# Kernel optimization log

Measured on AMD Instinct MI355X. Metric: run time of the kernel, lower is better.

## Reference

```python
import jax, jax.numpy as jnp
import numpy as np

HIDDEN = 2048
N_HEADS = 32
N_KV_HEADS = 8
HEAD_DIM = HIDDEN // N_HEADS  # 64
GROUPS = N_HEADS // N_KV_HEADS  # 4
ROPE_THETA = 10000.0
B, S = 1, 2048


def setup_inputs() -> dict:
    key = jax.random.key(0)
    ks = jax.random.split(key, 5)
    scale = 1.0 / np.sqrt(HIDDEN)
    return {
        "hidden_states": jax.random.normal(ks[0], (B, S, HIDDEN), dtype=jnp.float32),
        "Wq": jax.random.normal(ks[1], (HIDDEN, N_HEADS * HEAD_DIM), dtype=jnp.float32) * scale,
        "Wk": jax.random.normal(ks[2], (HIDDEN, N_KV_HEADS * HEAD_DIM), dtype=jnp.float32) * scale,
        "Wv": jax.random.normal(ks[3], (HIDDEN, N_KV_HEADS * HEAD_DIM), dtype=jnp.float32) * scale,
        "Wo": jax.random.normal(ks[4], (N_HEADS * HEAD_DIM, HIDDEN), dtype=jnp.float32) * scale,
    }


def _rope_tables(seq_len, dtype):
    # freqs_cos/sin buffers: [seq_len, HEAD_DIM//2]
    inv_freq = 1.0 / (ROPE_THETA ** (jnp.arange(0, HEAD_DIM, 2, dtype=jnp.float32) / HEAD_DIM))
    t = jnp.arange(seq_len, dtype=jnp.float32)
    freqs = jnp.outer(t, inv_freq)
    return jnp.cos(freqs).astype(dtype), jnp.sin(freqs).astype(dtype)


def _apply_rope(x, cos, sin):
    # x: [B, H, S, Dh], interleaved even/odd rotation
    xe = x[..., 0::2]
    xo = x[..., 1::2]
    # cos/sin: [S, Dh/2] -> broadcast over batch & heads
    out_e = xe * cos - xo * sin
    out_o = xe * sin + xo * cos
    return jnp.stack([out_e, out_o], axis=-1).reshape(x.shape)


def reference(hidden_states, Wq, Wk, Wv, Wo):
    bsz, q_len, _ = hidden_states.shape
    dtype = hidden_states.dtype

    q = (hidden_states @ Wq).reshape(bsz, q_len, N_HEADS, HEAD_DIM).transpose(0, 2, 1, 3)
    k = (hidden_states @ Wk).reshape(bsz, q_len, N_KV_HEADS, HEAD_DIM).transpose(0, 2, 1, 3)
    v = (hidden_states @ Wv).reshape(bsz, q_len, N_KV_HEADS, HEAD_DIM).transpose(0, 2, 1, 3)

    cos, sin = _rope_tables(q_len, dtype)
    q = _apply_rope(q, cos, sin)
    k = _apply_rope(k, cos, sin)

    # GQA: repeat_interleave kv heads to match query heads
    k = jnp.repeat(k, GROUPS, axis=1)  # [B, H, S, Dh]
    v = jnp.repeat(v, GROUPS, axis=1)

    # attention_mask=None path: no mask applied (matches module default)
    scores = jnp.einsum("bhqd,bhkd->bhqk", q, k) / jnp.sqrt(jnp.asarray(HEAD_DIM, dtype))
    attn = jax.nn.softmax(scores.astype(jnp.float32), axis=-1).astype(dtype)
    out = jnp.einsum("bhqk,bhkd->bhqd", attn, v)
    out = out.transpose(0, 2, 1, 3).reshape(bsz, q_len, N_HEADS * HEAD_DIM)
    return out @ Wo
```

## Files before the change

kernel.cpp:

```cpp
#include <hip/hip_runtime.h>

typedef __bf16 bf16x8 __attribute__((ext_vector_type(8)));
typedef float f32x4 __attribute__((ext_vector_type(4)));
typedef unsigned short u16x4 __attribute__((ext_vector_type(4)));
typedef unsigned short u16x8 __attribute__((ext_vector_type(8)));
typedef unsigned int u32x4 __attribute__((ext_vector_type(4)));

__device__ __forceinline__ float bf2f(unsigned short h) {
    union { unsigned int u; float f; } v;
    v.u = ((unsigned int)h) << 16;
    return v.f;
}
__device__ __forceinline__ unsigned short f2bf(float f) {
    return __builtin_bit_cast(unsigned short, (__bf16)f);
}
__device__ __forceinline__ void glds16(const unsigned short* g, unsigned short* l) {
    __builtin_amdgcn_global_load_lds((__attribute__((address_space(1))) void*)g,
                                     (__attribute__((address_space(3))) void*)l,
                                     16, 0, 0);
}

#define MFMA16(a, b, c) __builtin_amdgcn_mfma_f32_16x16x32_bf16((a), (b), (c), 0, 0, 0)

__global__ __launch_bounds__(256) void prep1(const float* __restrict__ X,
                                             const float* __restrict__ Wq,
                                             const float* __restrict__ Wk,
                                             const float* __restrict__ Wv,
                                             unsigned short* __restrict__ Xbf,
                                             unsigned short* __restrict__ wqkvT) {
    const int b = blockIdx.x;
    const int tid = threadIdx.x;
    if (b < 4096) {
        const int i = (b * 256 + tid) * 4;
        const float4 v = *(const float4*)(X + i);
        u16x4 o;
        o[0] = f2bf(v.x); o[1] = f2bf(v.y); o[2] = f2bf(v.z); o[3] = f2bf(v.w);
        *(u16x4*)(Xbf + i) = o;
        return;
    }
    __shared__ __align__(16) unsigned short tile[32][33];
    const int tx = tid & 31, ty = tid >> 5;
    const int b2 = b - 4096;
    const int kb = (b2 & 63) * 32;
    const int nb = (b2 >> 6) * 32;
    const float* src; int scol, sld;
    if (nb < 2048)      { src = Wq; scol = nb;        sld = 2048; }
    else if (nb < 2560) { src = Wk; scol = nb - 2048; sld = 512;  }
    else                { src = Wv; scol = nb - 2560; sld = 512;  }
#pragma unroll
    for (int i = 0; i < 32; i += 8)
        tile[ty + i][tx] = f2bf(src[(size_t)(kb + ty + i) * sld + (scol + tx)]);
    __syncthreads();
#pragma unroll
    for (int i = 0; i < 32; i += 8)
        wqkvT[(size_t)(nb + ty + i) * 2048 + (kb + tx)] = tile[tx][ty + i];
}

__global__ __launch_bounds__(256) void prep2(const float* __restrict__ Wo,
                                             const unsigned short* __restrict__ qkv,
                                             unsigned short* __restrict__ woT,
                                             unsigned short* __restrict__ vt) {
    const int b = blockIdx.x;
    const int tid = threadIdx.x;
    const int tx = tid & 31, ty = tid >> 5;
    __shared__ __align__(16) unsigned short tile[32][33];
    if (b < 4096) {
        const int kb = (b & 63) * 32;
        const int nb = (b >> 6) * 32;
#pragma unroll
        for (int i = 0; i < 32; i += 8)
            tile[ty + i][tx] = f2bf(Wo[(size_t)(kb + ty + i) * 2048 + (nb + tx)]);
        __syncthreads();
#pragma unroll
        for (int i = 0; i < 32; i += 8)
            woT[(size_t)(nb + ty + i) * 2048 + (kb + tx)] = tile[tx][ty + i];
    } else {
        const int b2 = b - 4096;
        const int bx = (b2 & 15) * 32;
        const int by = (b2 >> 4) * 32;
#pragma unroll
        for (int i = 0; i < 32; i += 8)
            tile[ty + i][tx] = qkv[(size_t)(by + ty + i) * 3072 + 2560 + bx + tx];
        __syncthreads();
#pragma unroll
        for (int i = 0; i < 32; i += 8)
            vt[(size_t)(bx + ty + i) * 2048 + (by + tx)] = tile[tx][ty + i];
    }
}

__global__ __launch_bounds__(256) void gemm128_qkv(const unsigned short* __restrict__ A,
                                                   const unsigned short* __restrict__ BT,
                                                   unsigned short* __restrict__ C) {
    __shared__ __align__(16) unsigned short As[128 * 64];
    __shared__ __align__(16) unsigned short Bs[128 * 64];

    const int tid = threadIdx.x;
    const int lane = tid & 63;
    const int wave = tid >> 6;
    const int quad = lane >> 4;
    const int l15 = lane & 15;
    const int bm = blockIdx.x * 128;
    const int bn = blockIdx.y * 128;
    const int wm = (wave & 1) * 64;
    const int wn = (wave >> 1) * 64;

    const int srow = wave * 8 + (lane >> 3);
    const int sw8 = (lane & 7) ^ (srow & 7);
    const unsigned short* Ag = A + (size_t)(bm + srow) * 2048 + sw8 * 8;
    const unsigned short* Bg = BT + (size_t)(bn + srow) * 2048 + sw8 * 8;
    unsigned short* Asl = As + wave * 512;
    unsigned short* Bsl = Bs + wave * 512;

    f32x4 acc[4][4] = {};

    for (int k0 = 0; k0 < 2048; k0 += 64) {
#pragma unroll
        for (int i = 0; i < 4; i++) {
            glds16(Ag + (size_t)(32 * i) * 2048 + k0, Asl + i * 2048);
            glds16(Bg + (size_t)(32 * i) * 2048 + k0, Bsl + i * 2048);
        }
        __syncthreads();
#pragma unroll
        for (int ks = 0; ks < 2; ks++) {
            bf16x8 af[4], bfr[4];
#pragma unroll
            for (int mt = 0; mt < 4; mt++) {
                const int row = wm + 16 * mt + l15;
                af[mt] = __builtin_bit_cast(bf16x8,
                    *(const u32x4*)&As[row * 64 + (((quad + 4 * ks) ^ (row & 7)) * 8)]);
            }
#pragma unroll
            for (int nt = 0; nt < 4; nt++) {
                const int row = wn + 16 * nt + l15;
                bfr[nt] = __builtin_bit_cast(bf16x8,
                    *(const u32x4*)&Bs[row * 64 + (((quad + 4 * ks) ^ (row & 7)) * 8)]);
            }
#pragma unroll
            for (int mt = 0; mt < 4; mt++)
#pragma unroll
                for (int nt = 0; nt < 4; nt++)
                    acc[mt][nt] = MFMA16(af[mt], bfr[nt], acc[mt][nt]);
        }
        __syncthreads();
    }

#pragma unroll
    for (int mt = 0; mt < 4; mt++) {
#pragma unroll
        for (int nt = 0; nt < 4; nt++) {
            const int col = bn + wn + 16 * nt + l15;
            if (col < 2560) {
                const int i = (col & 63) >> 1;
                const float inv = exp2f(-0.41524101186092036f * (float)i);
                const float sign = (col & 1) ? 1.0f : -1.0f;
#pragma unroll
                for (int r = 0; r < 4; r++) {
                    const int row = bm + wm + 16 * mt + quad * 4 + r;
                    float sn, cs;
                    __sincosf((float)row * inv, &sn, &cs);
                    const float partner = __shfl_xor(acc[mt][nt][r], 1, 64);
                    acc[mt][nt][r] = acc[mt][nt][r] * cs + sign * partner * sn;
                }
            }
#pragma unroll
            for (int r = 0; r < 4; r++) {
                const int row = bm + wm + 16 * mt + quad * 4 + r;
                C[(size_t)row * 3072 + col] = f2bf(acc[mt][nt][r]);
            }
        }
    }
}

template <int BM, bool ROPE>
__global__ __launch_bounds__(256) void gemm_bt(const unsigned short* __restrict__ A,
                                               const unsigned short* __restrict__ BT,
                                               void* __restrict__ Cv,
                                               int K, int lda, int ldb, int ldc,
                                               int out_f32) {
    constexpr int MT = BM / 32;
    constexpr int ACALLS = BM / 16;
    __shared__ __align__(16) unsigned short As[BM * 128];
    __shared__ __align__(16) unsigned short Bs[128 * 128];

    const int tid = threadIdx.x;
    const int lane = tid & 63;
    const int wave = tid >> 6;
    const int quad = lane >> 4;
    const int l15 = lane & 15;
    const int bm = blockIdx.x * BM;
    const int bn = blockIdx.y * 128;
    const int wm = (wave & 1) * (BM / 2);
    const int wn = (wave >> 1) * 64;

    const int srow = wave * 4 + (lane >> 4);
    const int sw = (lane & 15) ^ (srow & 7);
    const unsigned short* Ag = A + (size_t)(bm + srow) * lda + sw * 8;
    const unsigned short* Bg = BT + (size_t)(bn + srow) * ldb + sw * 8;
    unsigned short* Asl = As + wave * 512;
    unsigned short* Bsl = Bs + wave * 512;

    f32x4 acc[MT][4] = {};

    for (int k0 = 0; k0 < K; k0 += 128) {
#pragma unroll
        for (int i = 0; i < ACALLS; i++)
            glds16(Ag + (size_t)(16 * i) * lda + k0, Asl + i * 2048);
#pragma unroll
        for (int i = 0; i < 8; i++)
            glds16(Bg + (size_t)(16 * i) * ldb + k0, Bsl + i * 2048);
        __syncthreads();
#pragma unroll
        for (int ks = 0; ks < 4; ks++) {
            bf16x8 af[MT], bfr[4];
#pragma unroll
            for (int mt = 0; mt < MT; mt++) {
                const int row = wm + 16 * mt + l15;
                af[mt] = __builtin_bit_cast(bf16x8,
                    *(const u32x4*)&As[row * 128 + (((quad + 4 * ks) ^ (row & 7)) * 8)]);
            }
#pragma unroll
            for (int nt = 0; nt < 4; nt++) {
                const int row = wn + 16 * nt + l15;
                bfr[nt] = __builtin_bit_cast(bf16x8,
                    *(const u32x4*)&Bs[row * 128 + (((quad + 4 * ks) ^ (row & 7)) * 8)]);
            }
#pragma unroll
            for (int mt = 0; mt < MT; mt++)
#pragma unroll
                for (int nt = 0; nt < 4; nt++)
                    acc[mt][nt] = MFMA16(af[mt], bfr[nt], acc[mt][nt]);
        }
        __syncthreads();
    }

    if (ROPE) {
#pragma unroll
        for (int mt = 0; mt < MT; mt++) {
#pragma unroll
            for (int nt = 0; nt < 4; nt++) {
                const int col = bn + wn + 16 * nt + l15;
                if (col < 2560) {
                    const int i = (col & 63) >> 1;
                    const float inv = exp2f(-0.41524101186092036f * (float)i);
                    const float sign = (col & 1) ? 1.0f : -1.0f;
#pragma unroll
                    for (int r = 0; r < 4; r++) {
                        const int row = bm + wm + 16 * mt + quad * 4 + r;
                        float sn, cs;
                        __sincosf((float)row * inv, &sn, &cs);
                        const float partner = __shfl_xor(acc[mt][nt][r], 1, 64);
                        acc[mt][nt][r] = acc[mt][nt][r] * cs + sign * partner * sn;
                    }
                }
            }
        }
    }

#pragma unroll
    for (int mt = 0; mt < MT; mt++) {
#pragma unroll
        for (int nt = 0; nt < 4; nt++) {
#pragma unroll
            for (int r = 0; r < 4; r++) {
                const int row = bm + wm + 16 * mt + quad * 4 + r;
                const int col = bn + wn + 16 * nt + l15;
                if (out_f32)
                    ((float*)Cv)[(size_t)row * ldc + col] = acc[mt][nt][r];
                else
                    ((unsigned short*)Cv)[(size_t)row * ldc + col] = f2bf(acc[mt][nt][r]);
            }
        }
    }
}

__global__ __launch_bounds__(256) void attn_kernel(const unsigned short* __restrict__ qkv,
                                                   const unsigned short* __restrict__ vt,
                                                   unsigned short* __restrict__ attn_out) {
    const int qb = blockIdx.x;
    const int h = blockIdx.y;
    const int kvh = h >> 2;
    const int tid = threadIdx.x;
    const int lane = tid & 63;
    const int wave = tid >> 6;
    const int quad = lane >> 4;
    const int l15 = lane & 15;
    const int l7 = l15 & 7;
    const int w0 = qb * 64 + wave * 16;

    __shared__ __align__(16) unsigned short Ks[128 * 64];
    __shared__ __align__(16) unsigned short Vs[64 * 128];
    __shared__ __align__(16) unsigned short St[4][16][64];
    unsigned short (*Sw)[64] = St[wave];

    const int srow = wave * 8 + (lane >> 3);
    const int swK = (lane & 7) ^ (srow & 7);
    const unsigned short* Kg = qkv + 2048 + kvh * 64 + swK * 8;
    unsigned short* Ksl = Ks + wave * 512;
    const int vrow = wave * 4 + (lane >> 4);
    const int swV = (lane & 15) ^ (vrow & 7);
    const unsigned short* Vg = vt + (size_t)(kvh * 64 + vrow) * 2048 + swV * 8;
    unsigned short* Vsl = Vs + wave * 512;

    const float QSCALE = 0.18033688011111093f;
    bf16x8 qf[2];
#pragma unroll
    for (int ks = 0; ks < 2; ks++) {
        u32x4 raw = *(const u32x4*)&qkv[(size_t)(w0 + l15) * 3072 + h * 64 + quad * 8 + 32 * ks];
        u16x8 t = __builtin_bit_cast(u16x8, raw);
#pragma unroll
        for (int j = 0; j < 8; j++) t[j] = f2bf(bf2f(t[j]) * QSCALE);
        qf[ks] = __builtin_bit_cast(bf16x8, t);
    }

    bf16x8 ones;
#pragma unroll
    for (int j = 0; j < 8; j++) ones[j] = (__bf16)1.0f;

    f32x4 acc_o[4] = {};
    f32x4 acc_l = {};

    for (int kb2 = 0; kb2 < 16; kb2++) {
        const int kbase = kb2 * 128;
#pragma unroll
        for (int i = 0; i < 4; i++) {
            glds16(Kg + (size_t)(kbase + srow + 32 * i) * 3072, Ksl + i * 2048);
            glds16(Vg + (size_t)(16 * i) * 2048 + kbase, Vsl + i * 2048);
        }
        __syncthreads();

#pragma unroll
        for (int kh = 0; kh < 2; kh++) {
            f32x4 st[4] = {};
            __builtin_amdgcn_s_setprio(1);
#pragma unroll
            for (int n = 0; n < 4; n++) {
                const int row = kh * 64 + 16 * n + l15;
                const bf16x8 kf0 = __builtin_bit_cast(bf16x8,
                    *(const u32x4*)&Ks[row * 64 + ((quad ^ l7) * 8)]);
                const bf16x8 kf1 = __builtin_bit_cast(bf16x8,
                    *(const u32x4*)&Ks[row * 64 + (((quad + 4) ^ l7) * 8)]);
                st[n] = MFMA16(kf0, qf[0], st[n]);
                st[n] = MFMA16(kf1, qf[1], st[n]);
            }
            __builtin_amdgcn_s_setprio(0);

            const int gq = quad >> 1, oq = (quad & 1) * 4;
#pragma unroll
            for (int n = 0; n < 4; n++) {
                u16x4 pk;
#pragma unroll
                for (int r = 0; r < 4; r++)
                    pk[r] = f2bf(exp2f(st[n][r]));
                *(u16x4*)&Sw[l15][(((2 * n + gq) ^ l7) << 3) + oq] = pk;
            }

            const bf16x8 pf0 = __builtin_bit_cast(bf16x8,
                *(const u32x4*)&Sw[l15][(quad ^ l7) << 3]);
            const bf16x8 pf1 = __builtin_bit_cast(bf16x8,
                *(const u32x4*)&Sw[l15][((quad + 4) ^ l7) << 3]);

            __builtin_amdgcn_s_setprio(1);
            acc_l = MFMA16(pf0, ones, acc_l);
            acc_l = MFMA16(pf1, ones, acc_l);

#pragma unroll
            for (int nt = 0; nt < 4; nt++) {
                const int row = 16 * nt + l15;
                const int c0 = kh * 8 + (quad ^ l7);
                const int c1 = kh * 8 + ((quad + 4) ^ l7);
                const bf16x8 vf0 = __builtin_bit_cast(bf16x8, *(const u32x4*)&Vs[row * 128 + c0 * 8]);
                const bf16x8 vf1 = __builtin_bit_cast(bf16x8, *(const u32x4*)&Vs[row * 128 + c1 * 8]);
                acc_o[nt] = MFMA16(pf0, vf0, acc_o[nt]);
                acc_o[nt] = MFMA16(pf1, vf1, acc_o[nt]);
            }
            __builtin_amdgcn_s_setprio(0);
        }
        __syncthreads();
    }

    float linv[4];
#pragma unroll
    for (int r = 0; r < 4; r++) linv[r] = 1.0f / acc_l[r];
#pragma unroll
    for (int nt = 0; nt < 4; nt++)
#pragma unroll
        for (int r = 0; r < 4; r++)
            attn_out[(size_t)(w0 + quad * 4 + r) * 2048 + h * 64 + 16 * nt + l15] =
                f2bf(acc_o[nt][r] * linv[r]);
}

extern "C" void kernel_launch(void* const* d_in, const int* in_sizes, int n_in,
                              void* d_out, int out_size, void* d_ws, size_t ws_size,
                              hipStream_t stream) {
    (void)in_sizes; (void)n_in; (void)out_size; (void)ws_size;

    const float* X  = (const float*)d_in[0];
    const float* Wq = (const float*)d_in[1];
    const float* Wk = (const float*)d_in[2];
    const float* Wv = (const float*)d_in[3];
    const float* Wo = (const float*)d_in[4];

    unsigned short* ws16  = (unsigned short*)d_ws;
    unsigned short* Xbf   = ws16;
    unsigned short* wqkvT = ws16 + (size_t)4194304;
    unsigned short* qkv   = (unsigned short*)d_out;
    unsigned short* vt    = ws16;
    unsigned short* attnO = ws16 + (size_t)1048576;
    unsigned short* woT   = ws16 + (size_t)5242880;

    prep1<<<10240, 256, 0, stream>>>(X, Wq, Wk, Wv, Xbf, wqkvT);

    gemm128_qkv<<<dim3(16, 24), 256, 0, stream>>>(Xbf, wqkvT, qkv);

    prep2<<<5120, 256, 0, stream>>>(Wo, qkv, woT, vt);

    attn_kernel<<<dim3(32, 32), 256, 0, stream>>>(qkv, vt, attnO);

    gemm_bt<64, false><<<dim3(32, 16), 256, 0, stream>>>(attnO, woT, (void*)d_out, 2048, 2048, 2048, 2048, 1);
}
```

Measured before the change: 237.9 us.

## Double-buffer K/V tiles in LDS and prefetch next tile during compute

The attention kernel now stages K/V in two LDS buffers and issues the global-to-LDS loads for the next 128-key tile before computing the current one. It waits with an explicit vmcnt instead of a full syncthreads. The two 64-key halves are also merged into one pass, so all eight score tiles are computed before the exp and PV steps. This aims to hide global load latency, at the cost of doubled LDS use (lower occupancy) and more live registers.

```diff
diff --git a/kernel.cpp b/kernel.cpp
--- a/kernel.cpp
+++ b/kernel.cpp
@@ -287,19 +287,19 @@
     const int l7 = l15 & 7;
     const int w0 = qb * 64 + wave * 16;
 
-    __shared__ __align__(16) unsigned short Ks[128 * 64];
-    __shared__ __align__(16) unsigned short Vs[64 * 128];
-    __shared__ __align__(16) unsigned short St[4][16][64];
-    unsigned short (*Sw)[64] = St[wave];
+    __shared__ __align__(16) unsigned short Ks[2][128 * 64];
+    __shared__ __align__(16) unsigned short Vs[2][64 * 128];
+    __shared__ __align__(16) unsigned short St[4][16][128];
+    unsigned short (*Sw)[128] = St[wave];
 
     const int srow = wave * 8 + (lane >> 3);
     const int swK = (lane & 7) ^ (srow & 7);
     const unsigned short* Kg = qkv + 2048 + kvh * 64 + swK * 8;
-    unsigned short* Ksl = Ks + wave * 512;
+    unsigned short* Ksb = &Ks[0][0] + wave * 512;
     const int vrow = wave * 4 + (lane >> 4);
     const int swV = (lane & 15) ^ (vrow & 7);
     const unsigned short* Vg = vt + (size_t)(kvh * 64 + vrow) * 2048 + swV * 8;
-    unsigned short* Vsl = Vs + wave * 512;
+    unsigned short* Vsb = &Vs[0][0] + wave * 512;
 
     const float QSCALE = 0.18033688011111093f;
     bf16x8 qf[2];
@@ -319,64 +319,91 @@
     f32x4 acc_o[4] = {};
     f32x4 acc_l = {};
 
-    for (int kb2 = 0; kb2 < 16; kb2++) {
-        const int kbase = kb2 * 128;
-#pragma unroll
-        for (int i = 0; i < 4; i++) {
-            glds16(Kg + (size_t)(kbase + srow + 32 * i) * 3072, Ksl + i * 2048);
-            glds16(Vg + (size_t)(16 * i) * 2048 + kbase, Vsl + i * 2048);
-        }
-        __syncthreads();
-
-#pragma unroll
-        for (int kh = 0; kh < 2; kh++) {
-            f32x4 st[4] = {};
-            __builtin_amdgcn_s_setprio(1);
+#define STAGE_KV(kt, b) do {                                                      \
+        const size_t kb_ = (size_t)(kt) * 128;                                    \
+        _Pragma("unroll")                                                         \
+        for (int i_ = 0; i_ < 4; i_++) {                                          \
+            glds16(Kg + (kb_ + srow + 32 * i_) * 3072, Ksb + (b) * 8192 + i_ * 2048); \
+            glds16(Vg + (size_t)(16 * i_) * 2048 + kb_, Vsb + (b) * 8192 + i_ * 2048); \
+        }                                                                         \
+    } while (0)
+
+    STAGE_KV(0, 0);
+
+    for (int kt = 0; kt < 16; kt++) {
+        const int cur = kt & 1;
+        if (kt < 15) {
+            STAGE_KV(kt + 1, cur ^ 1);
+            asm volatile("s_waitcnt vmcnt(8)" ::: "memory");
+        } else {
+            asm volatile("s_waitcnt vmcnt(0)" ::: "memory");
+        }
+        __builtin_amdgcn_s_barrier();
+
+        const unsigned short* Kb = Ks[cur];
+        const unsigned short* Vb = Vs[cur];
+
+        f32x4 st[8] = {};
+        __builtin_amdgcn_s_setprio(1);
+#pragma unroll
+        for (int kh = 0; kh < 2; kh++)
 #pragma unroll
             for (int n = 0; n < 4; n++) {
                 const int row = kh * 64 + 16 * n + l15;
                 const bf16x8 kf0 = __builtin_bit_cast(bf16x8,
-                    *(const u32x4*)&Ks[row * 64 + ((quad ^ l7) * 8)]);
+                    *(const u32x4*)&Kb[row * 64 + ((quad ^ l7) * 8)]);
                 const bf16x8 kf1 = __builtin_bit_cast(bf16x8,
-                    *(const u32x4*)&Ks[row * 64 + (((quad + 4) ^ l7) * 8)]);
-                st[n] = MFMA16(kf0, qf[0], st[n]);
-                st[n] = MFMA16(kf1, qf[1], st[n]);
-            }
-            __builtin_amdgcn_s_setprio(0);
-
-            const int gq = quad >> 1, oq = (quad & 1) * 4;
+                    *(const u32x4*)&Kb[row * 64 + (((quad + 4) ^ l7) * 8)]);
+                st[kh * 4 + n] = MFMA16(kf0, qf[0], st[kh * 4 + n]);
+                st[kh * 4 + n] = MFMA16(kf1, qf[1], st[kh * 4 + n]);
+            }
+        __builtin_amdgcn_s_setprio(0);
+
+        const int gq = quad >> 1, oq = (quad & 1) * 4;
+#pragma unroll
+        for (int kh = 0; kh < 2; kh++)
 #pragma unroll
             for (int n = 0; n < 4; n++) {
                 u16x4 pk;
 #pragma unroll
                 for (int r = 0; r < 4; r++)
-                    pk[r] = f2bf(exp2f(st[n][r]));
-                *(u16x4*)&Sw[l15][(((2 * n + gq) ^ l7) << 3) + oq] = pk;
-            }
-
-            const bf16x8 pf0 = __builtin_bit_cast(bf16x8,
-                *(const u32x4*)&Sw[l15][(quad ^ l7) << 3]);
-            const bf16x8 pf1 = __builtin_bit_cast(bf16x8,
-                *(const u32x4*)&Sw[l15][((quad + 4) ^ l7) << 3]);
-
-            __builtin_amdgcn_s_setprio(1);
-            acc_l = MFMA16(pf0, ones, acc_l);
-            acc_l = MFMA16(pf1, ones, acc_l);
-
+                    pk[r] = f2bf(exp2f(st[kh * 4 + n][r]));
+                *(u16x4*)&Sw[l15][((kh * 8 + ((2 * n + gq) ^ l7)) << 3) + oq] = pk;
+            }
+
+        bf16x8 pf[2][2];
+#pragma unroll
+        for (int kh = 0; kh < 2; kh++) {
+            pf[kh][0] = __builtin_bit_cast(bf16x8,
+                *(const u32x4*)&Sw[l15][(kh * 8 + (quad ^ l7)) << 3]);
+            pf[kh][1] = __builtin_bit_cast(bf16x8,
+                *(const u32x4*)&Sw[l15][(kh * 8 + ((quad + 4) ^ l7)) << 3]);
+        }
+
+        __builtin_amdgcn_s_setprio(1);
+#pragma unroll
+        for (int kh = 0; kh < 2; kh++) {
+            acc_l = MFMA16(pf[kh][0], ones, acc_l);
+            acc_l = MFMA16(pf[kh][1], ones, acc_l);
+        }
+
+#pragma unroll
+        for (int kh = 0; kh < 2; kh++)
 #pragma unroll
             for (int nt = 0; nt < 4; nt++) {
                 const int row = 16 * nt + l15;
                 const int c0 = kh * 8 + (quad ^ l7);
                 const int c1 = kh * 8 + ((quad + 4) ^ l7);
-                const bf16x8 vf0 = __builtin_bit_cast(bf16x8, *(const u32x4*)&Vs[row * 128 + c0 * 8]);
-                const bf16x8 vf1 = __builtin_bit_cast(bf16x8, *(const u32x4*)&Vs[row * 128 + c1 * 8]);
-                acc_o[nt] = MFMA16(pf0, vf0, acc_o[nt]);
-                acc_o[nt] = MFMA16(pf1, vf1, acc_o[nt]);
-            }
-            __builtin_amdgcn_s_setprio(0);
-        }
-        __syncthreads();
-    }
+                const bf16x8 vf0 = __builtin_bit_cast(bf16x8, *(const u32x4*)&Vb[row * 128 + c0 * 8]);
+                const bf16x8 vf1 = __builtin_bit_cast(bf16x8, *(const u32x4*)&Vb[row * 128 + c1 * 8]);
+                acc_o[nt] = MFMA16(pf[kh][0], vf0, acc_o[nt]);
+                acc_o[nt] = MFMA16(pf[kh][1], vf1, acc_o[nt]);
+            }
+        __builtin_amdgcn_s_setprio(0);
+
+        __builtin_amdgcn_s_barrier();
+    }
+#undef STAGE_KV
 
     float linv[4];
 #pragma unroll
```

Result: slower. 244.1 us (+2.6%).

## Vectorize transpose prep kernels with 64x64 tiles and double attention query rows per wave

Applied to the files above, without the earlier changes.

The weight-transpose and V-transpose prep kernels now use 64x64 LDS tiles with float4 and 8-wide vector loads and 4-wide stores instead of scalar 32x32 tiles, which reduces the number of memory instructions and blocks. The attention kernel now has each wave handle two 16-row query tiles, so each K and V fragment read from LDS feeds twice as many MFMAs. This halves the grid to 16x32 blocks and halves the global loads of K/V. The cost is higher register pressure from doubled accumulators, and fewer blocks (512) relative to the CU count, which may lower occupancy.

```diff
diff --git a/kernel.cpp b/kernel.cpp
--- a/kernel.cpp
+++ b/kernel.cpp
@@ -38,22 +38,32 @@
         *(u16x4*)(Xbf + i) = o;
         return;
     }
-    __shared__ __align__(16) unsigned short tile[32][33];
-    const int tx = tid & 31, ty = tid >> 5;
+    __shared__ __align__(16) unsigned short Lt[64][72];
     const int b2 = b - 4096;
-    const int kb = (b2 & 63) * 32;
-    const int nb = (b2 >> 6) * 32;
+    const int kb = (b2 & 31) * 64;
+    const int nb = (b2 >> 5) * 64;
     const float* src; int scol, sld;
     if (nb < 2048)      { src = Wq; scol = nb;        sld = 2048; }
     else if (nb < 2560) { src = Wk; scol = nb - 2048; sld = 512;  }
     else                { src = Wv; scol = nb - 2560; sld = 512;  }
-#pragma unroll
-    for (int i = 0; i < 32; i += 8)
-        tile[ty + i][tx] = f2bf(src[(size_t)(kb + ty + i) * sld + (scol + tx)]);
+    const int r16 = tid >> 4, c4 = tid & 15;
+#pragma unroll
+    for (int i = 0; i < 4; i++) {
+        const int row = r16 + 16 * i;
+        const float4 v = *(const float4*)(src + (size_t)(kb + row) * sld + scol + c4 * 4);
+        u16x4 o;
+        o[0] = f2bf(v.x); o[1] = f2bf(v.y); o[2] = f2bf(v.z); o[3] = f2bf(v.w);
+        *(u16x4*)&Lt[row][c4 * 4] = o;
+    }
     __syncthreads();
 #pragma unroll
-    for (int i = 0; i < 32; i += 8)
-        wqkvT[(size_t)(nb + ty + i) * 2048 + (kb + tx)] = tile[tx][ty + i];
+    for (int i = 0; i < 4; i++) {
+        const int orow = r16 + 16 * i;
+        u16x4 o;
+#pragma unroll
+        for (int j = 0; j < 4; j++) o[j] = Lt[c4 * 4 + j][orow];
+        *(u16x4*)&wqkvT[(size_t)(nb + orow) * 2048 + kb + c4 * 4] = o;
+    }
 }
 
 __global__ __launch_bounds__(256) void prep2(const float* __restrict__ Wo,
@@ -62,29 +72,48 @@
                                              unsigned short* __restrict__ vt) {
     const int b = blockIdx.x;
     const int tid = threadIdx.x;
-    const int tx = tid & 31, ty = tid >> 5;
-    __shared__ __align__(16) unsigned short tile[32][33];
-    if (b < 4096) {
-        const int kb = (b & 63) * 32;
-        const int nb = (b >> 6) * 32;
-#pragma unroll
-        for (int i = 0; i < 32; i += 8)
-            tile[ty + i][tx] = f2bf(Wo[(size_t)(kb + ty + i) * 2048 + (nb + tx)]);
-        __syncthreads();
-#pragma unroll
-        for (int i = 0; i < 32; i += 8)
-            woT[(size_t)(nb + ty + i) * 2048 + (kb + tx)] = tile[tx][ty + i];
+    __shared__ __align__(16) unsigned short Lt[64][72];
+    const int r16 = tid >> 4, c4 = tid & 15;
+    if (b < 1024) {
+        const int kb = (b & 31) * 64;
+        const int nb = (b >> 5) * 64;
+#pragma unroll
+        for (int i = 0; i < 4; i++) {
+            const int row = r16 + 16 * i;
+            const float4 v = *(const float4*)(Wo + (size_t)(kb + row) * 2048 + nb + c4 * 4);
+            u16x4 o;
+            o[0] = f2bf(v.x); o[1] = f2bf(v.y); o[2] = f2bf(v.z); o[3] = f2bf(v.w);
+            *(u16x4*)&Lt[row][c4 * 4] = o;
+        }
+        __syncthreads();
+#pragma unroll
+        for (int i = 0; i < 4; i++) {
+            const int orow = r16 + 16 * i;
+            u16x4 o;
+#pragma unroll
+            for (int j = 0; j < 4; j++) o[j] = Lt[c4 * 4 + j][orow];
+            *(u16x4*)&woT[(size_t)(nb + orow) * 2048 + kb + c4 * 4] = o;
+        }
     } else {
-        const int b2 = b - 4096;
-        const int bx = (b2 & 15) * 32;
-        const int by = (b2 >> 4) * 32;
-#pragma unroll
-        for (int i = 0; i < 32; i += 8)
-            tile[ty + i][tx] = qkv[(size_t)(by + ty + i) * 3072 + 2560 + bx + tx];
-        __syncthreads();
-#pragma unroll
-        for (int i = 0; i < 32; i += 8)
-            vt[(size_t)(bx + ty + i) * 2048 + (by + tx)] = tile[tx][ty + i];
+        const int b2 = b - 1024;
+        const int bx = (b2 & 7) * 64;
+        const int by = (b2 >> 3) * 64;
+        const int r32 = tid >> 3, c8 = tid & 7;
+#pragma unroll
+        for (int i = 0; i < 2; i++) {
+            const int row = r32 + 32 * i;
+            *(u16x8*)&Lt[row][c8 * 8] =
+                *(const u16x8*)&qkv[(size_t)(by + row) * 3072 + 2560 + bx + c8 * 8];
+        }
+        __syncthreads();
+#pragma unroll
+        for (int i = 0; i < 4; i++) {
+            const int orow = r16 + 16 * i;
+            u16x4 o;
+#pragma unroll
+            for (int j = 0; j < 4; j++) o[j] = Lt[c4 * 4 + j][orow];
+            *(u16x4*)&vt[(size_t)(bx + orow) * 2048 + by + c4 * 4] = o;
+        }
     }
 }
 
@@ -284,13 +313,12 @@
     const int wave = tid >> 6;
     const int quad = lane >> 4;
     const int l15 = lane & 15;
-    const int l7 = l15 & 7;
-    const int w0 = qb * 64 + wave * 16;
+    const int w0 = qb * 128 + wave * 32;
 
     __shared__ __align__(16) unsigned short Ks[128 * 64];
     __shared__ __align__(16) unsigned short Vs[64 * 128];
-    __shared__ __align__(16) unsigned short St[4][16][64];
-    unsigned short (*Sw)[64] = St[wave];
+    __shared__ __align__(16) unsigned short St[4][32][72];
+    unsigned short (*Sw)[72] = St[wave];
 
     const int srow = wave * 8 + (lane >> 3);
     const int swK = (lane & 7) ^ (srow & 7);
@@ -302,22 +330,24 @@
     unsigned short* Vsl = Vs + wave * 512;
 
     const float QSCALE = 0.18033688011111093f;
-    bf16x8 qf[2];
-#pragma unroll
-    for (int ks = 0; ks < 2; ks++) {
-        u32x4 raw = *(const u32x4*)&qkv[(size_t)(w0 + l15) * 3072 + h * 64 + quad * 8 + 32 * ks];
-        u16x8 t = __builtin_bit_cast(u16x8, raw);
-#pragma unroll
-        for (int j = 0; j < 8; j++) t[j] = f2bf(bf2f(t[j]) * QSCALE);
-        qf[ks] = __builtin_bit_cast(bf16x8, t);
-    }
+    bf16x8 qf[2][2];
+#pragma unroll
+    for (int mt = 0; mt < 2; mt++)
+#pragma unroll
+        for (int ks = 0; ks < 2; ks++) {
+            u32x4 raw = *(const u32x4*)&qkv[(size_t)(w0 + 16 * mt + l15) * 3072 + h * 64 + quad * 8 + 32 * ks];
+            u16x8 t = __builtin_bit_cast(u16x8, raw);
+#pragma unroll
+            for (int j = 0; j < 8; j++) t[j] = f2bf(bf2f(t[j]) * QSCALE);
+            qf[mt][ks] = __builtin_bit_cast(bf16x8, t);
+        }
 
     bf16x8 ones;
 #pragma unroll
     for (int j = 0; j < 8; j++) ones[j] = (__bf16)1.0f;
 
-    f32x4 acc_o[4] = {};
-    f32x4 acc_l = {};
+    f32x4 acc_o[2][4] = {};
+    f32x4 acc_l[2] = {};
 
     for (int kb2 = 0; kb2 < 16; kb2++) {
         const int kbase = kb2 * 128;
@@ -330,63 +360,78 @@
 
 #pragma unroll
         for (int kh = 0; kh < 2; kh++) {
-            f32x4 st[4] = {};
+            f32x4 st[2][4] = {};
             __builtin_amdgcn_s_setprio(1);
 #pragma unroll
             for (int n = 0; n < 4; n++) {
                 const int row = kh * 64 + 16 * n + l15;
                 const bf16x8 kf0 = __builtin_bit_cast(bf16x8,
-                    *(const u32x4*)&Ks[row * 64 + ((quad ^ l7) * 8)]);
+                    *(const u32x4*)&Ks[row * 64 + ((quad ^ (l15 & 7)) * 8)]);
                 const bf16x8 kf1 = __builtin_bit_cast(bf16x8,
-                    *(const u32x4*)&Ks[row * 64 + (((quad + 4) ^ l7) * 8)]);
-                st[n] = MFMA16(kf0, qf[0], st[n]);
-                st[n] = MFMA16(kf1, qf[1], st[n]);
+                    *(const u32x4*)&Ks[row * 64 + (((quad + 4) ^ (l15 & 7)) * 8)]);
+#pragma unroll
+                for (int mt = 0; mt < 2; mt++) {
+                    st[mt][n] = MFMA16(kf0, qf[mt][0], st[mt][n]);
+                    st[mt][n] = MFMA16(kf1, qf[mt][1], st[mt][n]);
+                }
             }
             __builtin_amdgcn_s_setprio(0);
 
-            const int gq = quad >> 1, oq = (quad & 1) * 4;
-#pragma unroll
-            for (int n = 0; n < 4; n++) {
-                u16x4 pk;
-#pragma unroll
-                for (int r = 0; r < 4; r++)
-                    pk[r] = f2bf(exp2f(st[n][r]));
-                *(u16x4*)&Sw[l15][(((2 * n + gq) ^ l7) << 3) + oq] = pk;
-            }
-
-            const bf16x8 pf0 = __builtin_bit_cast(bf16x8,
-                *(const u32x4*)&Sw[l15][(quad ^ l7) << 3]);
-            const bf16x8 pf1 = __builtin_bit_cast(bf16x8,
-                *(const u32x4*)&Sw[l15][((quad + 4) ^ l7) << 3]);
+#pragma unroll
+            for (int mt = 0; mt < 2; mt++)
+#pragma unroll
+                for (int n = 0; n < 4; n++) {
+                    u16x4 pk;
+#pragma unroll
+                    for (int r = 0; r < 4; r++)
+                        pk[r] = f2bf(exp2f(st[mt][n][r]));
+                    *(u16x4*)&Sw[16 * mt + l15][16 * n + quad * 4] = pk;
+                }
+
+            bf16x8 pf[2][2];
+#pragma unroll
+            for (int mt = 0; mt < 2; mt++) {
+                pf[mt][0] = __builtin_bit_cast(bf16x8, *(const u32x4*)&Sw[16 * mt + l15][quad * 8]);
+                pf[mt][1] = __builtin_bit_cast(bf16x8, *(const u32x4*)&Sw[16 * mt + l15][quad * 8 + 32]);
+            }
 
             __builtin_amdgcn_s_setprio(1);
-            acc_l = MFMA16(pf0, ones, acc_l);
-            acc_l = MFMA16(pf1, ones, acc_l);
+#pragma unroll
+            for (int mt = 0; mt < 2; mt++) {
+                acc_l[mt] = MFMA16(pf[mt][0], ones, acc_l[mt]);
+                acc_l[mt] = MFMA16(pf[mt][1], ones, acc_l[mt]);
+            }
 
 #pragma unroll
             for (int nt = 0; nt < 4; nt++) {
                 const int row = 16 * nt + l15;
-                const int c0 = kh * 8 + (quad ^ l7);
-                const int c1 = kh * 8 + ((quad + 4) ^ l7);
+                const int c0 = kh * 8 + (quad ^ (l15 & 7));
+                const int c1 = kh * 8 + ((quad + 4) ^ (l15 & 7));
                 const bf16x8 vf0 = __builtin_bit_cast(bf16x8, *(const u32x4*)&Vs[row * 128 + c0 * 8]);
                 const bf16x8 vf1 = __builtin_bit_cast(bf16x8, *(const u32x4*)&Vs[row * 128 + c1 * 8]);
-                acc_o[nt] = MFMA16(pf0, vf0, acc_o[nt]);
-                acc_o[nt] = MFMA16(pf1, vf1, acc_o[nt]);
+#pragma unroll
+                for (int mt = 0; mt < 2; mt++) {
+                    acc_o[mt][nt] = MFMA16(pf[mt][0], vf0, acc_o[mt][nt]);
+                    acc_o[mt][nt] = MFMA16(pf[mt][1], vf1, acc_o[mt][nt]);
+                }
             }
             __builtin_amdgcn_s_setprio(0);
         }
         __syncthreads();
     }
 
-    float linv[4];
-#pragma unroll
-    for (int r = 0; r < 4; r++) linv[r] = 1.0f / acc_l[r];
-#pragma unroll
-    for (int nt = 0; nt < 4; nt++)
-#pragma unroll
-        for (int r = 0; r < 4; r++)
-            attn_out[(size_t)(w0 + quad * 4 + r) * 2048 + h * 64 + 16 * nt + l15] =
-                f2bf(acc_o[nt][r] * linv[r]);
+#pragma unroll
+    for (int mt = 0; mt < 2; mt++) {
+        float linv[4];
+#pragma unroll
+        for (int r = 0; r < 4; r++) linv[r] = 1.0f / acc_l[mt][r];
+#pragma unroll
+        for (int nt = 0; nt < 4; nt++)
+#pragma unroll
+            for (int r = 0; r < 4; r++)
+                attn_out[(size_t)(w0 + 16 * mt + quad * 4 + r) * 2048 + h * 64 + 16 * nt + l15] =
+                    f2bf(acc_o[mt][nt][r] * linv[r]);
+    }
 }
 
 extern "C" void kernel_launch(void* const* d_in, const int* in_sizes, int n_in,
@@ -408,13 +453,13 @@
     unsigned short* attnO = ws16 + (size_t)1048576;
     unsigned short* woT   = ws16 + (size_t)5242880;
 
-    prep1<<<10240, 256, 0, stream>>>(X, Wq, Wk, Wv, Xbf, wqkvT);
+    prep1<<<5632, 256, 0, stream>>>(X, Wq, Wk, Wv, Xbf, wqkvT);
 
     gemm128_qkv<<<dim3(16, 24), 256, 0, stream>>>(Xbf, wqkvT, qkv);
 
-    prep2<<<5120, 256, 0, stream>>>(Wo, qkv, woT, vt);
-
-    attn_kernel<<<dim3(32, 32), 256, 0, stream>>>(qkv, vt, attnO);
+    prep2<<<1280, 256, 0, stream>>>(Wo, qkv, woT, vt);
+
+    attn_kernel<<<dim3(16, 32), 256, 0, stream>>>(qkv, vt, attnO);
 
     gemm_bt<64, false><<<dim3(32, 16), 256, 0, stream>>>(attnO, woT, (void*)d_out, 2048, 2048, 2048, 2048, 1);
 }
```

Result: faster. 232.8 us (-2.1%).
